# Kernel optimization log

Measured on AMD Instinct MI355X. Metric: run time of the kernel, lower is better.

Reference implementation:

```python
import jax, jax.numpy as jnp
import numpy as np

E = 400000
N = 100000
B = 64
D = 128          # token_dim
H = 128          # hidden_dim
A = 2 * H        # action_dim


def setup_inputs() -> dict:
    key = jax.random.key(0)
    ks = jax.random.split(key, 12)
    inp = {
        "relation_tokens": jax.random.normal(ks[0], (E, D), jnp.float32),
        "node_tokens": jax.random.normal(ks[1], (N, D), jnp.float32),
        "edge_index": jax.random.randint(ks[2], (2, E), 0, N, jnp.int64 if jax.config.jax_enable_x64 else jnp.int32),
        "question_tokens": jax.random.normal(ks[3], (B, D), jnp.float32),
        "edge_batch": jax.random.randint(ks[4], (E,), 0, B, jnp.int64 if jax.config.jax_enable_x64 else jnp.int32),
        # learned params (xavier-like small init); stored as [in, out] for x @ W
        "W_rel": jax.random.normal(ks[5], (D, H), jnp.float32) * 0.05,
        "W_node": jax.random.normal(ks[6], (D, H), jnp.float32) * 0.05,
        "W_qgate": jax.random.normal(ks[7], (D, A), jnp.float32) * 0.05,
        "W_mlp1": jax.random.normal(ks[8], (A, A), jnp.float32) * 0.05,
        "b_mlp1": jnp.zeros((A,), jnp.float32),
        "W_mlp2": jax.random.normal(ks[9], (A, A), jnp.float32) * 0.05,
        "b_mlp2": jnp.zeros((A,), jnp.float32),
    }
    return inp


def reference(relation_tokens, node_tokens, edge_index, question_tokens, edge_batch,
              W_rel, W_node, W_qgate, W_mlp1, b_mlp1, W_mlp2, b_mlp2):
    # TrajectoryAgent.precompute_action_keys (dropout=0 -> identity)
    tail_nodes = edge_index[1]                       # [E]
    tail_tokens = node_tokens[tail_nodes]            # gather -> [E, D]
    q_tokens = question_tokens[edge_batch]           # gather -> [E, D]

    rel_key = relation_tokens @ W_rel                # [E, H]
    node_key = tail_tokens @ W_node                  # [E, H]
    q_gate = jax.nn.sigmoid(q_tokens @ W_qgate)      # [E, 2H]

    action_key = jnp.concatenate((rel_key, node_key), axis=-1) * q_gate  # [E, 2H]

    # action_mlp: Linear -> exact GELU -> Linear (torch nn.GELU default = erf)
    h = jax.nn.gelu(action_key @ W_mlp1 + b_mlp1, approximate=False)
    return h @ W_mlp2 + b_mlp2                       # [E, 2H]
```

## Files before the change

kernel.cpp:

```cpp
#include <hip/hip_runtime.h>

typedef __bf16 bf16;
typedef bf16 bf16x4 __attribute__((ext_vector_type(4)));
typedef bf16 bf16x8 __attribute__((ext_vector_type(8)));
typedef float f32x4 __attribute__((ext_vector_type(4)));

#define WS_PK1   0
#define WS_PK2   32768
#define WS_PK3   98304
#define WS_QG_F  163840

__global__ void prep_weights(const float* __restrict__ Wrel,
                             const float* __restrict__ Wnode,
                             const float* __restrict__ W1,
                             const float* __restrict__ W2,
                             bf16* __restrict__ ws) {
  int id = blockIdx.x * 256 + threadIdx.x;
  if (id < 32768) {
    int cg = id >> 13, rem = id & 8191;
    int kk = rem >> 11;
    int ai = (rem >> 9) & 3;
    int l  = (rem >> 3) & 63;
    int j  = rem & 7;
    int n  = (cg & 1) * 64 + ai * 16 + (l & 15);
    int k  = kk * 32 + (l >> 4) * 8 + j;
    const float* src = (cg >> 1) ? Wnode : Wrel;
    ws[WS_PK1 + id] = (bf16)src[k * 128 + n];
  } else if (id < 98304) {
    int t = id - 32768;
    int cg = t >> 14, rem = t & 16383;
    int kk = rem >> 11;
    int ai = (rem >> 9) & 3;
    int l  = (rem >> 3) & 63;
    int j  = rem & 7;
    int n  = cg * 64 + ai * 16 + (l & 15);
    int k  = kk * 32 + (l >> 4) * 8 + j;
    ws[WS_PK2 + t] = (bf16)W1[k * 256 + n];
  } else if (id < 163840) {
    int t = id - 98304;
    int cg = t >> 14, rem = t & 16383;
    int kk = rem >> 11;
    int ai = (rem >> 9) & 3;
    int l  = (rem >> 3) & 63;
    int j  = rem & 7;
    int n  = cg * 64 + ai * 16 + (l & 15);
    int k  = kk * 32 + (l >> 4) * 8 + j;
    ws[WS_PK3 + t] = (bf16)W2[k * 256 + n];
  }
}

__global__ void prep_qg(const float* __restrict__ question,
                        const float* __restrict__ Wq,
                        float* __restrict__ qgf) {
  int b = blockIdx.x, c = threadIdx.x;
  float s = 0.f;
#pragma unroll 8
  for (int k = 0; k < 128; ++k) s += question[b * 128 + k] * Wq[k * 256 + c];
  qgf[b * 256 + c] = 1.f / (1.f + expf(-s));
}

__device__ __forceinline__ float gelu_fast(float x) {
  float m = x * x;
  float t = fmaf(0.10294537f, m, 2.30220790f);
  float e = __builtin_amdgcn_exp2f(t * x);
  float r = __builtin_amdgcn_rcpf(e + 1.f);
  return x - x * r;
}

typedef __attribute__((address_space(1))) const void gq_t;
typedef __attribute__((address_space(3))) void lq_t;
#define GLD16(g, s) __builtin_amdgcn_global_load_lds((gq_t*)(g), (lq_t*)(s), 16, 0, 0)
#define SB() __builtin_amdgcn_sched_barrier(0xF)
#define WAIT_VM4()   { asm volatile("s_waitcnt vmcnt(4)" ::: "memory"); SB(); }
#define WAIT_VM0()   { asm volatile("s_waitcnt vmcnt(0)" ::: "memory"); SB(); }
#define WAIT_LGKM0() { asm volatile("s_waitcnt lgkmcnt(0)" ::: "memory"); SB(); }
#define BAR() __builtin_amdgcn_s_barrier()

__global__ __launch_bounds__(256, 2) void fused_main(
    const float* __restrict__ rel_tok,
    const float* __restrict__ node_tok,
    const int*   __restrict__ tail_idx,
    const int*   __restrict__ ebatch,
    const bf16*  __restrict__ pk1,
    const bf16*  __restrict__ pk2,
    const bf16*  __restrict__ pk3,
    const float* __restrict__ qgf,
    const float* __restrict__ b1,
    const float* __restrict__ b2,
    float* __restrict__ out)
{
  __shared__ char  s_buf[32768];
  __shared__ char  s_w[32768];
  __shared__ float s_bias[512];

  const int tid = threadIdx.x;
  const int cg  = tid >> 6;
  const int l   = tid & 63;
  const int lo  = l & 15;
  const int hi  = l >> 4;
  const int base = blockIdx.x * 64;
  const int h1  = cg >> 1;

  auto issue_step = [&](int s) {
    const bf16* g;
    if (s < 4)       g = pk1 + cg * 8192  + s * 2048;
    else if (s < 12) g = pk2 + cg * 16384 + (s - 4) * 2048;
    else             g = pk3 + cg * 16384 + (s - 12) * 2048;
    g += l * 8;
    char* d = s_w + (s & 1) * 16384 + cg * 4096;
#pragma unroll
    for (int ai = 0; ai < 4; ++ai) GLD16(g + ai * 512, d + ai * 1024);
  };

  int ebv[4];
#pragma unroll
  for (int bj = 0; bj < 4; ++bj) ebv[bj] = ebatch[base + bj * 16 + lo];
  float4 gv[4][4];
#pragma unroll
  for (int bj = 0; bj < 4; ++bj)
#pragma unroll
    for (int ai = 0; ai < 4; ++ai)
      gv[bj][ai] = *(const float4*)(qgf + ebv[bj] * 256 + cg * 64 + ai * 16 + hi * 4);
  s_bias[tid]       = b1[tid];
  s_bias[256 + tid] = b2[tid];

  {
    const float4* g = (const float4*)rel_tok + (size_t)base * 32;
#pragma unroll
    for (int i = 0; i < 8; ++i) {
      int idx = tid + i * 256;
      int row = idx >> 5, c4 = idx & 31;
      float4 v = g[idx];
      bf16x4 b; b[0] = (bf16)v.x; b[1] = (bf16)v.y; b[2] = (bf16)v.z; b[3] = (bf16)v.w;
      int off = row * 256 + ((c4 * 8) ^ ((row & 15) << 4));
      *(bf16x4*)(s_buf + off) = b;
    }
#pragma unroll
    for (int i = 0; i < 8; ++i) {
      int idx = tid + i * 256;
      int row = idx >> 5, c4 = idx & 31;
      int tail = tail_idx[base + row];
      float4 v = ((const float4*)node_tok)[(size_t)tail * 32 + c4];
      bf16x4 b; b[0] = (bf16)v.x; b[1] = (bf16)v.y; b[2] = (bf16)v.z; b[3] = (bf16)v.w;
      int off = 16384 + row * 256 + ((c4 * 8) ^ ((row & 15) << 4));
      *(bf16x4*)(s_buf + off) = b;
    }
  }

  WAIT_VM0();
  issue_step(0);
  issue_step(1);
  WAIT_LGKM0();
  BAR();

  const f32x4 zero4 = {0.f, 0.f, 0.f, 0.f};
  const int wb = cg * 4096 + l * 16;

  f32x4 acc1[4][4];
#pragma unroll
  for (int ai = 0; ai < 4; ++ai)
#pragma unroll
    for (int bj = 0; bj < 4; ++bj) acc1[ai][bj] = zero4;

#pragma unroll
  for (int kk = 0; kk < 4; ++kk) {
    const int s = kk;
    WAIT_VM4();
    bf16x8 a[4];
#pragma unroll
    for (int ai = 0; ai < 4; ++ai)
      a[ai] = *(const bf16x8*)(s_w + (s & 1) * 16384 + wb + ai * 1024);
    WAIT_LGKM0();
    issue_step(s + 2);
    __builtin_amdgcn_s_setprio(1);
#pragma unroll
    for (int bj = 0; bj < 4; ++bj) {
      int e = bj * 16 + lo;
      bf16x8 b = *(const bf16x8*)(s_buf + h1 * 16384 + e * 256 +
                                  ((kk * 64 + hi * 16) ^ ((e & 15) << 4)));
#pragma unroll
      for (int ai = 0; ai < 4; ++ai)
        acc1[ai][bj] = __builtin_amdgcn_mfma_f32_16x16x32_bf16(a[ai], b, acc1[ai][bj], 0, 0, 0);
    }
    __builtin_amdgcn_s_setprio(0);
  }
  BAR();

#pragma unroll
  for (int bj = 0; bj < 4; ++bj) {
    int e = bj * 16 + lo;
#pragma unroll
    for (int ai = 0; ai < 4; ++ai) {
      int col0 = cg * 64 + ai * 16 + hi * 4;
      bf16x4 pk;
      pk[0] = (bf16)(acc1[ai][bj][0] * gv[bj][ai].x);
      pk[1] = (bf16)(acc1[ai][bj][1] * gv[bj][ai].y);
      pk[2] = (bf16)(acc1[ai][bj][2] * gv[bj][ai].z);
      pk[3] = (bf16)(acc1[ai][bj][3] * gv[bj][ai].w);
      int off = e * 512 + ((2 * col0) ^ ((e & 15) << 4));
      *(bf16x4*)(s_buf + off) = pk;
    }
  }
  WAIT_LGKM0();
  BAR();

  f32x4 acc2[4][4];
#pragma unroll
  for (int ai = 0; ai < 4; ++ai)
#pragma unroll
    for (int bj = 0; bj < 4; ++bj) acc2[ai][bj] = zero4;

#pragma unroll
  for (int kk = 0; kk < 8; ++kk) {
    const int s = 4 + kk;
    WAIT_VM4();
    bf16x8 a[4];
#pragma unroll
    for (int ai = 0; ai < 4; ++ai)
      a[ai] = *(const bf16x8*)(s_w + (s & 1) * 16384 + wb + ai * 1024);
    WAIT_LGKM0();
    issue_step(s + 2);
    __builtin_amdgcn_s_setprio(1);
#pragma unroll
    for (int bj = 0; bj < 4; ++bj) {
      int e = bj * 16 + lo;
      bf16x8 b = *(const bf16x8*)(s_buf + e * 512 +
                                  ((kk * 64 + hi * 16) ^ ((e & 15) << 4)));
#pragma unroll
      for (int ai = 0; ai < 4; ++ai)
        acc2[ai][bj] = __builtin_amdgcn_mfma_f32_16x16x32_bf16(a[ai], b, acc2[ai][bj], 0, 0, 0);
    }
    __builtin_amdgcn_s_setprio(0);
  }
  BAR();

#pragma unroll
  for (int bj = 0; bj < 4; ++bj) {
    int e = bj * 16 + lo;
#pragma unroll
    for (int ai = 0; ai < 4; ++ai) {
      int col0 = cg * 64 + ai * 16 + hi * 4;
      float4 bv = *(const float4*)(s_bias + col0);
      bf16x4 pk;
      pk[0] = (bf16)gelu_fast(acc2[ai][bj][0] + bv.x);
      pk[1] = (bf16)gelu_fast(acc2[ai][bj][1] + bv.y);
      pk[2] = (bf16)gelu_fast(acc2[ai][bj][2] + bv.z);
      pk[3] = (bf16)gelu_fast(acc2[ai][bj][3] + bv.w);
      int off = e * 512 + ((2 * col0) ^ ((e & 15) << 4));
      *(bf16x4*)(s_buf + off) = pk;
    }
  }
  WAIT_LGKM0();
  BAR();

  f32x4 acc3[4][4];
#pragma unroll
  for (int ai = 0; ai < 4; ++ai)
#pragma unroll
    for (int bj = 0; bj < 4; ++bj) acc3[ai][bj] = zero4;

#pragma unroll
  for (int kk = 0; kk < 8; ++kk) {
    const int s = 12 + kk;
    if (s < 19) { WAIT_VM4(); } else { WAIT_VM0(); }
    bf16x8 a[4];
#pragma unroll
    for (int ai = 0; ai < 4; ++ai)
      a[ai] = *(const bf16x8*)(s_w + (s & 1) * 16384 + wb + ai * 1024);
    WAIT_LGKM0();
    if (s + 2 <= 19) issue_step(s + 2);
    __builtin_amdgcn_s_setprio(1);
#pragma unroll
    for (int bj = 0; bj < 4; ++bj) {
      int e = bj * 16 + lo;
      bf16x8 b = *(const bf16x8*)(s_buf + e * 512 +
                                  ((kk * 64 + hi * 16) ^ ((e & 15) << 4)));
#pragma unroll
      for (int ai = 0; ai < 4; ++ai)
        acc3[ai][bj] = __builtin_amdgcn_mfma_f32_16x16x32_bf16(a[ai], b, acc3[ai][bj], 0, 0, 0);
    }
    __builtin_amdgcn_s_setprio(0);
  }

#pragma unroll
  for (int bj = 0; bj < 4; ++bj) {
    int e = bj * 16 + lo;
#pragma unroll
    for (int ai = 0; ai < 4; ++ai) {
      int col0 = cg * 64 + ai * 16 + hi * 4;
      float4 bv = *(const float4*)(s_bias + 256 + col0);
      float4 o;
      o.x = acc3[ai][bj][0] + bv.x;
      o.y = acc3[ai][bj][1] + bv.y;
      o.z = acc3[ai][bj][2] + bv.z;
      o.w = acc3[ai][bj][3] + bv.w;
      *(float4*)(out + (size_t)(base + e) * 256 + col0) = o;
    }
  }
}

extern "C" void kernel_launch(void* const* d_in, const int* in_sizes, int n_in,
                              void* d_out, int out_size, void* d_ws, size_t ws_size,
                              hipStream_t stream) {
  const float* rel    = (const float*)d_in[0];
  const float* node   = (const float*)d_in[1];
  const int*   eidx   = (const int*)d_in[2];
  const float* quest  = (const float*)d_in[3];
  const int*   ebat   = (const int*)d_in[4];
  const float* Wrel   = (const float*)d_in[5];
  const float* Wnode  = (const float*)d_in[6];
  const float* Wq     = (const float*)d_in[7];
  const float* W1     = (const float*)d_in[8];
  const float* bias1  = (const float*)d_in[9];
  const float* W2     = (const float*)d_in[10];
  const float* bias2  = (const float*)d_in[11];
  float* outp = (float*)d_out;
  bf16* ws = (bf16*)d_ws;
  float* qgf = (float*)(ws + WS_QG_F);

  const int E = in_sizes[4];

  prep_weights<<<640, 256, 0, stream>>>(Wrel, Wnode, W1, W2, ws);
  prep_qg<<<64, 256, 0, stream>>>(quest, Wq, qgf);
  fused_main<<<E / 64, 256, 0, stream>>>(
      rel, node, eidx + E, ebat,
      ws + WS_PK1, ws + WS_PK2, ws + WS_PK3, qgf,
      bias1, bias2, outp);
}
```

Baseline: 278.9 us.

## Split fused kernel into three stage kernels with bf16 intermediate in workspace

Adds a three-kernel path (gate-scaled action-key GEMM, MLP1+GELU, MLP2) that stores the bf16 intermediate activations in a large workspace buffer. It is used only when the workspace is large enough, otherwise the fused kernel still runs. The aim is lower register and LDS pressure per kernel, allowing three blocks per CU. The cost is about 200 MB of extra global memory traffic for writing and re-reading the intermediate, plus two extra launches.

```diff
diff --git a/kernel.cpp b/kernel.cpp
--- a/kernel.cpp
+++ b/kernel.cpp
@@ -5,10 +5,13 @@
 typedef bf16 bf16x8 __attribute__((ext_vector_type(8)));
 typedef float f32x4 __attribute__((ext_vector_type(4)));
 
-#define WS_PK1   0
-#define WS_PK2   32768
-#define WS_PK3   98304
-#define WS_QG_F  163840
+#define WS_PK1    0
+#define WS_PK2    32768
+#define WS_PK3    98304
+#define WS_QG     163840
+#define WS_QGF_B  180224
+#define WS_AKH    212992
+#define WS_SPLIT_BYTES (425984ull + 204800000ull)
 
 __global__ void prep_weights(const float* __restrict__ Wrel,
                              const float* __restrict__ Wnode,
@@ -51,12 +54,15 @@
 
 __global__ void prep_qg(const float* __restrict__ question,
                         const float* __restrict__ Wq,
-                        float* __restrict__ qgf) {
+                        float* __restrict__ qgf,
+                        bf16* __restrict__ qg) {
   int b = blockIdx.x, c = threadIdx.x;
   float s = 0.f;
 #pragma unroll 8
   for (int k = 0; k < 128; ++k) s += question[b * 128 + k] * Wq[k * 256 + c];
-  qgf[b * 256 + c] = 1.f / (1.f + expf(-s));
+  float v = 1.f / (1.f + expf(-s));
+  qgf[b * 256 + c] = v;
+  qg[b * 256 + c]  = (bf16)v;
 }
 
 __device__ __forceinline__ float gelu_fast(float x) {
@@ -75,6 +81,204 @@
 #define WAIT_VM0()   { asm volatile("s_waitcnt vmcnt(0)" ::: "memory"); SB(); }
 #define WAIT_LGKM0() { asm volatile("s_waitcnt lgkmcnt(0)" ::: "memory"); SB(); }
 #define BAR() __builtin_amdgcn_s_barrier()
+
+__global__ __launch_bounds__(256, 3) void k1_ak(
+    const float* __restrict__ rel_tok,
+    const float* __restrict__ node_tok,
+    const int*   __restrict__ tail_idx,
+    const int*   __restrict__ ebatch,
+    const bf16*  __restrict__ pk1,
+    const bf16*  __restrict__ qg,
+    bf16* __restrict__ akh)
+{
+  __shared__ char s_tok[32768];
+  const int tid = threadIdx.x;
+  const int cg = tid >> 6, l = tid & 63, lo = l & 15, hi = l >> 4;
+  const int base = blockIdx.x * 64;
+  const int h1 = cg >> 1;
+
+  int ebv[4];
+#pragma unroll
+  for (int bj = 0; bj < 4; ++bj) ebv[bj] = ebatch[base + bj * 16 + lo];
+  bf16x4 gv[4][4];
+#pragma unroll
+  for (int bj = 0; bj < 4; ++bj)
+#pragma unroll
+    for (int ai = 0; ai < 4; ++ai)
+      gv[bj][ai] = *(const bf16x4*)(qg + ebv[bj] * 256 + cg * 64 + ai * 16 + hi * 4);
+
+  {
+    const float4* g = (const float4*)rel_tok + (size_t)base * 32;
+#pragma unroll
+    for (int i = 0; i < 8; ++i) {
+      int idx = tid + i * 256;
+      int row = idx >> 5, c4 = idx & 31;
+      float4 v = g[idx];
+      bf16x4 b; b[0] = (bf16)v.x; b[1] = (bf16)v.y; b[2] = (bf16)v.z; b[3] = (bf16)v.w;
+      int off = row * 256 + ((c4 * 8) ^ ((row & 15) << 4));
+      *(bf16x4*)(s_tok + off) = b;
+    }
+#pragma unroll
+    for (int i = 0; i < 8; ++i) {
+      int idx = tid + i * 256;
+      int row = idx >> 5, c4 = idx & 31;
+      int tail = tail_idx[base + row];
+      float4 v = ((const float4*)node_tok)[(size_t)tail * 32 + c4];
+      bf16x4 b; b[0] = (bf16)v.x; b[1] = (bf16)v.y; b[2] = (bf16)v.z; b[3] = (bf16)v.w;
+      int off = 16384 + row * 256 + ((c4 * 8) ^ ((row & 15) << 4));
+      *(bf16x4*)(s_tok + off) = b;
+    }
+  }
+  __syncthreads();
+
+  const f32x4 zero4 = {0.f, 0.f, 0.f, 0.f};
+  f32x4 acc[4][4];
+#pragma unroll
+  for (int ai = 0; ai < 4; ++ai)
+#pragma unroll
+    for (int bj = 0; bj < 4; ++bj) acc[ai][bj] = zero4;
+
+#pragma unroll
+  for (int kk = 0; kk < 4; ++kk) {
+    bf16x8 a[4];
+#pragma unroll
+    for (int ai = 0; ai < 4; ++ai)
+      a[ai] = *(const bf16x8*)(pk1 + cg * 8192 + (kk * 4 + ai) * 512 + l * 8);
+#pragma unroll
+    for (int bj = 0; bj < 4; ++bj) {
+      int e = bj * 16 + lo;
+      bf16x8 b = *(const bf16x8*)(s_tok + h1 * 16384 + e * 256 +
+                                  ((kk * 64 + hi * 16) ^ ((e & 15) << 4)));
+#pragma unroll
+      for (int ai = 0; ai < 4; ++ai)
+        acc[ai][bj] = __builtin_amdgcn_mfma_f32_16x16x32_bf16(a[ai], b, acc[ai][bj], 0, 0, 0);
+    }
+  }
+
+#pragma unroll
+  for (int bj = 0; bj < 4; ++bj) {
+    int e = bj * 16 + lo;
+#pragma unroll
+    for (int ai = 0; ai < 4; ++ai) {
+      int col0 = cg * 64 + ai * 16 + hi * 4;
+      bf16x4 pk;
+      pk[0] = (bf16)(acc[ai][bj][0] * (float)gv[bj][ai][0]);
+      pk[1] = (bf16)(acc[ai][bj][1] * (float)gv[bj][ai][1]);
+      pk[2] = (bf16)(acc[ai][bj][2] * (float)gv[bj][ai][2]);
+      pk[3] = (bf16)(acc[ai][bj][3] * (float)gv[bj][ai][3]);
+      *(bf16x4*)(akh + (size_t)(base + e) * 256 + col0) = pk;
+    }
+  }
+}
+
+__global__ __launch_bounds__(256, 3) void k2_mlp1(
+    bf16* __restrict__ akh,
+    const bf16* __restrict__ pk2,
+    const float* __restrict__ b1)
+{
+  const int tid = threadIdx.x;
+  const int cg = tid >> 6, l = tid & 63, lo = l & 15, hi = l >> 4;
+  const int base = blockIdx.x * 64;
+
+  float4 b1v[4];
+#pragma unroll
+  for (int ai = 0; ai < 4; ++ai)
+    b1v[ai] = *(const float4*)(b1 + cg * 64 + ai * 16 + hi * 4);
+
+  const f32x4 zero4 = {0.f, 0.f, 0.f, 0.f};
+  f32x4 acc[4][4];
+#pragma unroll
+  for (int ai = 0; ai < 4; ++ai)
+#pragma unroll
+    for (int bj = 0; bj < 4; ++bj) acc[ai][bj] = zero4;
+
+#pragma unroll
+  for (int kk = 0; kk < 8; ++kk) {
+    bf16x8 a[4];
+#pragma unroll
+    for (int ai = 0; ai < 4; ++ai)
+      a[ai] = *(const bf16x8*)(pk2 + cg * 16384 + (kk * 4 + ai) * 512 + l * 8);
+#pragma unroll
+    for (int bj = 0; bj < 4; ++bj) {
+      int e = bj * 16 + lo;
+      bf16x8 b = *(const bf16x8*)(akh + (size_t)(base + e) * 256 + kk * 32 + hi * 8);
+#pragma unroll
+      for (int ai = 0; ai < 4; ++ai)
+        acc[ai][bj] = __builtin_amdgcn_mfma_f32_16x16x32_bf16(a[ai], b, acc[ai][bj], 0, 0, 0);
+    }
+  }
+  asm volatile("s_waitcnt vmcnt(0)" ::: "memory");
+  __syncthreads();
+
+#pragma unroll
+  for (int bj = 0; bj < 4; ++bj) {
+    int e = bj * 16 + lo;
+#pragma unroll
+    for (int ai = 0; ai < 4; ++ai) {
+      int col0 = cg * 64 + ai * 16 + hi * 4;
+      bf16x4 pk;
+      pk[0] = (bf16)gelu_fast(acc[ai][bj][0] + b1v[ai].x);
+      pk[1] = (bf16)gelu_fast(acc[ai][bj][1] + b1v[ai].y);
+      pk[2] = (bf16)gelu_fast(acc[ai][bj][2] + b1v[ai].z);
+      pk[3] = (bf16)gelu_fast(acc[ai][bj][3] + b1v[ai].w);
+      *(bf16x4*)(akh + (size_t)(base + e) * 256 + col0) = pk;
+    }
+  }
+}
+
+__global__ __launch_bounds__(256, 3) void k3_mlp2(
+    const bf16* __restrict__ akh,
+    const bf16* __restrict__ pk3,
+    const float* __restrict__ b2,
+    float* __restrict__ out)
+{
+  const int tid = threadIdx.x;
+  const int cg = tid >> 6, l = tid & 63, lo = l & 15, hi = l >> 4;
+  const int base = blockIdx.x * 64;
+
+  float4 b2v[4];
+#pragma unroll
+  for (int ai = 0; ai < 4; ++ai)
+    b2v[ai] = *(const float4*)(b2 + cg * 64 + ai * 16 + hi * 4);
+
+  const f32x4 zero4 = {0.f, 0.f, 0.f, 0.f};
+  f32x4 acc[4][4];
+#pragma unroll
+  for (int ai = 0; ai < 4; ++ai)
+#pragma unroll
+    for (int bj = 0; bj < 4; ++bj) acc[ai][bj] = zero4;
+
+#pragma unroll
+  for (int kk = 0; kk < 8; ++kk) {
+    bf16x8 a[4];
+#pragma unroll
+    for (int ai = 0; ai < 4; ++ai)
+      a[ai] = *(const bf16x8*)(pk3 + cg * 16384 + (kk * 4 + ai) * 512 + l * 8);
+#pragma unroll
+    for (int bj = 0; bj < 4; ++bj) {
+      int e = bj * 16 + lo;
+      bf16x8 b = *(const bf16x8*)(akh + (size_t)(base + e) * 256 + kk * 32 + hi * 8);
+#pragma unroll
+      for (int ai = 0; ai < 4; ++ai)
+        acc[ai][bj] = __builtin_amdgcn_mfma_f32_16x16x32_bf16(a[ai], b, acc[ai][bj], 0, 0, 0);
+    }
+  }
+
+#pragma unroll
+  for (int bj = 0; bj < 4; ++bj) {
+    int e = bj * 16 + lo;
+#pragma unroll
+    for (int ai = 0; ai < 4; ++ai) {
+      int col0 = cg * 64 + ai * 16 + hi * 4;
+      float4 o;
+      o.x = acc[ai][bj][0] + b2v[ai].x;
+      o.y = acc[ai][bj][1] + b2v[ai].y;
+      o.z = acc[ai][bj][2] + b2v[ai].z;
+      o.w = acc[ai][bj][3] + b2v[ai].w;
+      *(float4*)(out + (size_t)(base + e) * 256 + col0) = o;
+    }
+  }
+}
 
 __global__ __launch_bounds__(256, 2) void fused_main(
     const float* __restrict__ rel_tok,
@@ -316,14 +520,23 @@
   const float* bias2  = (const float*)d_in[11];
   float* outp = (float*)d_out;
   bf16* ws = (bf16*)d_ws;
-  float* qgf = (float*)(ws + WS_QG_F);
+  float* qgf = (float*)(ws + WS_QGF_B);
+  bf16* akh = ws + WS_AKH;
 
   const int E = in_sizes[4];
 
   prep_weights<<<640, 256, 0, stream>>>(Wrel, Wnode, W1, W2, ws);
-  prep_qg<<<64, 256, 0, stream>>>(quest, Wq, qgf);
-  fused_main<<<E / 64, 256, 0, stream>>>(
-      rel, node, eidx + E, ebat,
-      ws + WS_PK1, ws + WS_PK2, ws + WS_PK3, qgf,
-      bias1, bias2, outp);
-}
+  prep_qg<<<64, 256, 0, stream>>>(quest, Wq, qgf, ws + WS_QG);
+
+  if (ws_size >= WS_SPLIT_BYTES) {
+    k1_ak<<<E / 64, 256, 0, stream>>>(rel, node, eidx + E, ebat,
+                                      ws + WS_PK1, ws + WS_QG, akh);
+    k2_mlp1<<<E / 64, 256, 0, stream>>>(akh, ws + WS_PK2, bias1);
+    k3_mlp2<<<E / 64, 256, 0, stream>>>(akh, ws + WS_PK3, bias2, outp);
+  } else {
+    fused_main<<<E / 64, 256, 0, stream>>>(
+        rel, node, eidx + E, ebat,
+        ws + WS_PK1, ws + WS_PK2, ws + WS_PK3, qgf,
+        bias1, bias2, outp);
+  }
+}
```

Measured after the change: 609.6 us. 119% more time.
